# Optimization experiments

Hardware: AMD Instinct MI355X
Metric: run time of the kernel (lower is better)

Reference implementation:

```python
import jax, jax.numpy as jnp
import numpy as np

B, L, D, H = 2, 2048, 2048, 16
HD = D // H          # head_dim = 128
LAT = HD // 4        # latent_dim = 32


def setup_inputs() -> dict:
    key = jax.random.key(0)
    ks = jax.random.split(key, 16)
    def w(k, shape, fan_in):
        return jax.random.normal(k, shape, jnp.float32) / np.float32(np.sqrt(fan_in))
    x = jax.random.normal(ks[0], (B, L, D), jnp.float32)
    # RoPE frequencies, stored as (cos, sin) pairs: [L, HD//2, 2]
    inv_freq = 1.0 / (10000.0 ** (np.arange(0, HD, 2, dtype=np.float32) / HD))
    ang = np.outer(np.arange(L, dtype=np.float32), inv_freq)
    freqs_cis = jnp.stack([jnp.asarray(np.cos(ang)), jnp.asarray(np.sin(ang))], axis=-1)
    return dict(
        x=x, freqs_cis=freqs_cis,
        Wq=w(ks[1], (D, D), D), bq=jnp.zeros((D,), jnp.float32),
        Wk=w(ks[2], (D, D), D), bk=jnp.zeros((D,), jnp.float32),
        Wv=w(ks[3], (D, D), D), bv=jnp.zeros((D,), jnp.float32),
        Wqc=w(ks[4], (LAT, HD), HD), bqc=jnp.zeros((LAT,), jnp.float32),
        Wkc=w(ks[5], (LAT, HD), HD), bkc=jnp.zeros((LAT,), jnp.float32),
        Wvc=w(ks[6], (LAT, HD), HD), bvc=jnp.zeros((LAT,), jnp.float32),
        Wd=w(ks[7], (HD, LAT), LAT), bd=jnp.zeros((HD,), jnp.float32),
        Wo=w(ks[8], (D, D), D), bo=jnp.zeros((D,), jnp.float32),
    )


def _rope(t, freqs_cis):
    # t: [B,H,L,HD]; freqs_cis: [L, HD//2, 2] (cos, sin)
    tp = t.reshape(t.shape[:-1] + (HD // 2, 2))
    a, b = tp[..., 0], tp[..., 1]
    cr = freqs_cis[:, :, 0]  # [L, HD//2]
    ci = freqs_cis[:, :, 1]
    ra = a * cr - b * ci
    rb = a * ci + b * cr
    return jnp.stack([ra, rb], axis=-1).reshape(t.shape)


def reference(x, freqs_cis, Wq, bq, Wk, bk, Wv, bv, Wqc, bqc, Wkc, bkc, Wvc, bvc, Wd, bd, Wo, bo):
    Bx, Lx, Dx = x.shape
    # QKV projections -> [B,H,L,HD]
    def proj(W, bias):
        return (x @ W.T + bias).reshape(Bx, Lx, H, HD).transpose(0, 2, 1, 3)
    q = proj(Wq, bq)
    k = proj(Wk, bk)
    v = proj(Wv, bv)
    q = _rope(q, freqs_cis)
    k = _rope(k, freqs_cis)
    # per-head compression to latent dim: [B,H,L,LAT]
    qc = q @ Wqc.T + bqc
    kc = k @ Wkc.T + bkc
    vc = v @ Wvc.T + bvc
    scores = jnp.einsum('bhie,bhje->bhij', qc, kc) / np.float32(np.sqrt(LAT))
    mask = jnp.triu(jnp.ones((Lx, Lx), bool), 1)  # future positions
    scores = jnp.where(mask, jnp.float32(-jnp.inf), scores)
    probs = jax.nn.softmax(scores, axis=-1)
    attn = jnp.einsum('bhij,bhje->bhie', probs, vc)  # [B,H,L,LAT]
    attn = attn @ Wd.T + bd                          # decompress -> [B,H,L,HD]
    attn = attn.transpose(0, 2, 1, 3).reshape(Bx, Lx, Dx)
    return attn @ Wo.T + bo
```

## Files before the change

### kernel.cpp

```cpp
#include <hip/hip_runtime.h>

typedef __attribute__((ext_vector_type(8))) __bf16 bf16x8;
typedef __attribute__((ext_vector_type(4))) __bf16 bf16x4;
typedef __attribute__((ext_vector_type(4))) float f32x4;
typedef __attribute__((ext_vector_type(16))) float f32x16;

#define LL 2048
#define DD 2048
#define HH 16
#define HDIM 128

__global__ __launch_bounds__(256)
void cvt_all(const float* __restrict__ x, const float* __restrict__ Wq,
             const float* __restrict__ Wk, const float* __restrict__ Wqc,
             const float* __restrict__ Wkc,
             __bf16* __restrict__ xb, __bf16* __restrict__ Wqb, __bf16* __restrict__ Wkb,
             __bf16* __restrict__ Wqcb, __bf16* __restrict__ Wkcb)
{
    size_t i = (size_t)blockIdx.x * 256 + threadIdx.x;
    const float* s; __bf16* d; size_t off;
    if (i < 2097152)      { s = x;   d = xb;   off = i; }
    else if (i < 3145728) { s = Wq;  d = Wqb;  off = i - 2097152; }
    else if (i < 4194304) { s = Wk;  d = Wkb;  off = i - 3145728; }
    else if (i < 4195328) { s = Wqc; d = Wqcb; off = i - 4194304; }
    else                  { s = Wkc; d = Wkcb; off = i - 4195328; }
    float4 v = *(const float4*)(s + off * 4);
    bf16x4 o = { (__bf16)v.x, (__bf16)v.y, (__bf16)v.z, (__bf16)v.w };
    *(bf16x4*)(d + off * 4) = o;
}

__global__ __launch_bounds__(256)
void build_wv_eff(const float* __restrict__ Wv, const float* __restrict__ Wvc,
                  const float* __restrict__ bv, const float* __restrict__ bvc,
                  __bf16* __restrict__ Wveff, float* __restrict__ bveff)
{
    __shared__ float WvcT[128][32];
    const int h = blockIdx.x, dc = blockIdx.y, tid = threadIdx.x;
    for (int i = tid; i < 4096; i += 256) WvcT[i & 127][i >> 7] = Wvc[i];
    __syncthreads();
    const int d  = dc * 64 + (tid & 63);
    const int o0 = (tid >> 6) * 8;
    float acc[8] = {};
    for (int j = 0; j < 128; ++j) {
        const float w = Wv[(size_t)(h * 128 + j) * 2048 + d];
        #pragma unroll
        for (int o = 0; o < 8; ++o) acc[o] += WvcT[j][o0 + o] * w;
    }
    #pragma unroll
    for (int o = 0; o < 8; ++o)
        Wveff[(size_t)(h * 32 + o0 + o) * 2048 + d] = (__bf16)acc[o];
    if (dc == 0 && tid < 32) {
        float s = bvc[tid];
        for (int j = 0; j < 128; ++j) s += WvcT[j][tid] * bv[h * 128 + j];
        bveff[h * 32 + tid] = s;
    }
}

__global__ __launch_bounds__(256)
void build_wo_eff(const float* __restrict__ Wo, const float* __restrict__ Wd,
                  __bf16* __restrict__ Woeff)
{
    __shared__ float WdL[128][32];
    const int dc = blockIdx.x, h = blockIdx.y, tid = threadIdx.x;
    for (int i = tid; i < 4096; i += 256) WdL[i >> 5][i & 31] = Wd[i];
    __syncthreads();
    const int dout = dc * 64 + (tid & 63);
    const int o0   = (tid >> 6) * 8;
    float acc[8] = {};
    const float* wrow = Wo + (size_t)dout * 2048 + h * 128;
    for (int u = 0; u < 128; ++u) {
        const float w = wrow[u];
        #pragma unroll
        for (int o = 0; o < 8; ++o) acc[o] += WdL[u][o0 + o] * w;
    }
    #pragma unroll
    for (int o = 0; o < 8; ++o)
        Woeff[(size_t)dout * 512 + h * 32 + o0 + o] = (__bf16)acc[o];
}

__global__ __launch_bounds__(256)
void build_bo_eff(const float* __restrict__ Wo, const float* __restrict__ bd,
                  const float* __restrict__ bo, float* __restrict__ boeff)
{
    __shared__ float bdL[128];
    const int tid = threadIdx.x;
    if (tid < 128) bdL[tid] = bd[tid];
    __syncthreads();
    const int d  = blockIdx.x * 32 + (tid >> 3);
    const int s0 = (tid & 7) * 64;
    float s = 0.f;
    const float* wrow = Wo + (size_t)d * 2048 + s0 * 4;
    for (int c4 = 0; c4 < 64; ++c4) {
        float4 wv = *(const float4*)(wrow + c4 * 4);
        const int cb = ((s0 + c4) * 4) & 127;
        s += wv.x * bdL[cb] + wv.y * bdL[cb + 1] + wv.z * bdL[cb + 2] + wv.w * bdL[cb + 3];
    }
    #pragma unroll
    for (int off = 4; off; off >>= 1) s += __shfl_down(s, off, 8);
    if ((tid & 7) == 0) boeff[d] = bo[d] + s;
}

typedef unsigned int u32;
typedef const __attribute__((address_space(1))) u32* gp_t;
typedef __attribute__((address_space(3))) u32* lp_t;
__device__ __forceinline__ void gload16(const __bf16* g, __bf16* l)
{
    __builtin_amdgcn_global_load_lds((gp_t)(const void*)g, (lp_t)(void*)l, 16, 0, 0);
}

#define MF16(a, b, c) __builtin_amdgcn_mfma_f32_16x16x32_bf16(a, b, c, 0, 0, 0)

__global__ __launch_bounds__(512, 2)
void gemm_qkv8(const __bf16* __restrict__ A,
               const __bf16* __restrict__ Wq, const __bf16* __restrict__ Wk,
               const __bf16* __restrict__ Wveff,
               const float* __restrict__ bq, const float* __restrict__ bk,
               const float* __restrict__ bveff,
               __bf16* __restrict__ qb, __bf16* __restrict__ kb, __bf16* __restrict__ vt)
{
    __shared__ __bf16 lds[2][4][8192];

    const int bid = blockIdx.x;
    const int xcd = bid & 7;
    const int jj  = bid >> 3;
    const int by  = xcd * 2 + (jj / 18);
    const int bx  = jj % 18;
    const int m0  = by * 256;
    const int which = (bx >= 16) ? 2 : (bx >> 3);
    const int nseg  = (which == 2) ? (bx - 16) * 256 : (bx & 7) * 256;
    const __bf16* W = which == 0 ? Wq : which == 1 ? Wk : Wveff;

    const int tid  = threadIdx.x;
    const int wid  = tid >> 6;
    const int lane = tid & 63;
    const int wr   = wid >> 2;
    const int wc   = wid & 3;
    const int l15  = lane & 15;
    const int l4   = lane >> 4;
    const int c7   = l15 & 7;
    const int slotB = 2 + (wc >> 1);
    const int rbB   = (wc & 1) * 64;

    const int r0 = tid >> 3;
    const int cs = ((tid & 7) ^ (r0 & 7)) * 8;

    const __bf16* gA0 = A + (size_t)(m0 + r0) * 2048 + cs;
    const __bf16* gB0 = W + (size_t)(nseg + r0) * 2048 + cs;

    #define STAGE_ALL(dbuf, kk)                                                \
    {                                                                          \
        __bf16* s0 = &lds[dbuf][0][wid * 512];                                 \
        __bf16* s1 = &lds[dbuf][1][wid * 512];                                 \
        __bf16* s2 = &lds[dbuf][2][wid * 512];                                 \
        __bf16* s3 = &lds[dbuf][3][wid * 512];                                 \
        gload16(gA0 + (kk), s0);                                               \
        gload16(gA0 + (size_t)64 * 2048 + (kk), s0 + 4096);                    \
        gload16(gA0 + (size_t)128 * 2048 + (kk), s1);                          \
        gload16(gA0 + (size_t)192 * 2048 + (kk), s1 + 4096);                   \
        gload16(gB0 + (kk), s2);                                               \
        gload16(gB0 + (size_t)64 * 2048 + (kk), s2 + 4096);                    \
        gload16(gB0 + (size_t)128 * 2048 + (kk), s3);                          \
        gload16(gB0 + (size_t)192 * 2048 + (kk), s3 + 4096);                   \
    }

    #define RD_A(dbuf, mf, ks) \
        (*(const bf16x8*)&lds[dbuf][wr][((mf) * 16 + l15) * 64 + ((((ks) * 4 + l4) ^ c7) * 8)])
    #define RD_B(dbuf, nf, ks) \
        (*(const bf16x8*)&lds[dbuf][slotB][(rbB + (nf) * 16 + l15) * 64 + ((((ks) * 4 + l4) ^ c7) * 8)])

    f32x4 acc[8][4] = {};

    STAGE_ALL(0, 0)
    __syncthreads();

    for (int t = 0; t < 32; ++t) {
        const int d  = t & 1;
        const int dn = d ^ 1;
        if (t < 31) STAGE_ALL(dn, (t + 1) * 64)

        #pragma unroll
        for (int ks = 0; ks < 2; ++ks) {
            bf16x8 fa[8], fb[4];
            #pragma unroll
            for (int mf = 0; mf < 8; ++mf) fa[mf] = RD_A(d, mf, ks);
            #pragma unroll
            for (int nf = 0; nf < 4; ++nf) fb[nf] = RD_B(d, nf, ks);
            __builtin_amdgcn_s_setprio(1);
            #pragma unroll
            for (int mf = 0; mf < 8; ++mf)
                #pragma unroll
                for (int nf = 0; nf < 4; ++nf)
                    acc[mf][nf] = MF16(fa[mf], fb[nf], acc[mf][nf]);
            __builtin_amdgcn_s_setprio(0);
        }
        __syncthreads();
    }
    #undef STAGE_ALL
    #undef RD_A
    #undef RD_B

    if (which < 2) {
        __bf16* C = which ? kb : qb;
        const float* bb = which ? bk : bq;
        #pragma unroll
        for (int nf = 0; nf < 4; ++nf) {
            const int col = nseg + wc * 64 + nf * 16 + l15;
            const float bv = bb[col];
            #pragma unroll
            for (int mf = 0; mf < 8; ++mf) {
                const int row0 = m0 + wr * 128 + mf * 16 + l4 * 4;
                #pragma unroll
                for (int rr = 0; rr < 4; ++rr)
                    C[(size_t)(row0 + rr) * 2048 + col] = (__bf16)(acc[mf][nf][rr] + bv);
            }
        }
    } else {
        #pragma unroll
        for (int nf = 0; nf < 4; ++nf) {
            const int ncol = nseg + wc * 64 + nf * 16 + l15;
            const float bv = bveff[ncol];
            const int hh = ncol >> 5, oo = ncol & 31;
            #pragma unroll
            for (int mf = 0; mf < 8; ++mf) {
                const int row0 = m0 + wr * 128 + mf * 16 + l4 * 4;
                const int b = row0 >> 11, l0 = row0 & 2047;
                bf16x4 pk = { (__bf16)(acc[mf][nf][0] + bv), (__bf16)(acc[mf][nf][1] + bv),
                              (__bf16)(acc[mf][nf][2] + bv), (__bf16)(acc[mf][nf][3] + bv) };
                *(bf16x4*)(vt + ((size_t)((b * 16 + hh) * 32 + oo)) * 2048 + l0) = pk;
            }
        }
    }
}

__global__ __launch_bounds__(256)
void gemm_ao(const __bf16* __restrict__ ao, const __bf16* __restrict__ Woeff,
             const float* __restrict__ boeff, float* __restrict__ out)
{
    __shared__ __bf16 As[128][64];
    __shared__ __bf16 Bs[128][64];
    const int bid = blockIdx.x;
    const int x   = bid & 7;
    const int jj  = bid >> 3;
    const int bx  = x * 2 + (jj & 1);
    const int by  = jj >> 1;
    const int m0  = by * 128;
    const int n0  = bx * 128;

    const int tid  = threadIdx.x;
    const int wave = tid >> 6;
    const int lane = tid & 63;
    const int wr   = (wave >> 1) * 64;
    const int wc   = (wave & 1) * 64;
    const int lr   = lane & 15;
    const int lk   = (lane >> 4) * 8;
    const int srow = wave * 32 + (lane >> 3);
    const int scol = (lane & 7) * 8;

    f32x4 acc[4][4] = {};
    __bf16* lA = &As[wave * 32][0];
    __bf16* lB = &Bs[wave * 32][0];
    const __bf16* Ww = Woeff + (size_t)(n0 + srow) * 512 + scol;

    for (int k0 = 0; k0 < 512; k0 += 64) {
        const int kk = k0 + scol;
        const int hblk = kk >> 5, oo = kk & 31;
        #pragma unroll
        for (int j = 0; j < 4; ++j) {
            const int r = m0 + srow + j * 8;
            const int b = r >> 11, l = r & 2047;
            gload16(ao + ((size_t)((b << 4) + hblk) * 2048 + l) * 32 + oo, lA + j * 512);
            gload16(Ww + (size_t)(j * 8) * 512 + k0, lB + j * 512);
        }
        __syncthreads();
        #pragma unroll
        for (int ks = 0; ks < 2; ++ks) {
            bf16x8 af[4], bfr[4];
            #pragma unroll
            for (int m = 0; m < 4; ++m)
                af[m] = *(const bf16x8*)(&As[wr + m * 16 + lr][ks * 32 + lk]);
            #pragma unroll
            for (int n = 0; n < 4; ++n)
                bfr[n] = *(const bf16x8*)(&Bs[wc + n * 16 + lr][ks * 32 + lk]);
            #pragma unroll
            for (int m = 0; m < 4; ++m)
                #pragma unroll
                for (int n = 0; n < 4; ++n)
                    acc[m][n] = MF16(af[m], bfr[n], acc[m][n]);
        }
        __syncthreads();
    }

    const int orow = (lane >> 4) * 4;
    #pragma unroll
    for (int n = 0; n < 4; ++n) {
        const int col = n0 + wc + n * 16 + lr;
        const float bv = boeff[col];
        #pragma unroll
        for (int m = 0; m < 4; ++m) {
            #pragma unroll
            for (int r = 0; r < 4; ++r) {
                const int row = m0 + wr + m * 16 + orow + r;
                out[(size_t)row * 2048 + col] = acc[m][n][r] + bv;
            }
        }
    }
}

__global__ __launch_bounds__(256)
void latproj_mfma(const __bf16* __restrict__ qb, const __bf16* __restrict__ kb,
                  const __bf16* __restrict__ Wqcb, const __bf16* __restrict__ Wkcb,
                  const float* __restrict__ bq, const float* __restrict__ bk,
                  const float* __restrict__ fc,
                  __bf16* __restrict__ qc, __bf16* __restrict__ kc)
{
    const int which = blockIdx.y;
    const __bf16* in = which == 0 ? qb : kb;
    const __bf16* Wb = which == 0 ? Wqcb : Wkcb;
    const float*  bs = which == 0 ? bq : bk;

    const int wave = threadIdx.x >> 6;
    const int lane = threadIdx.x & 63;
    const int o    = lane & 31;
    const int hi   = lane >> 5;
    const int g0   = (blockIdx.x * 4 + wave) * 32;

    bf16x8 wf[8];
    #pragma unroll
    for (int ks = 0; ks < 8; ++ks)
        wf[ks] = *(const bf16x8*)(Wb + o * 128 + ks * 16 + hi * 8);

    const int g = g0 + o;
    const int b = g >> 15, h = (g >> 11) & 15, l = g & (LL - 1);
    const __bf16* arow = in + ((size_t)(b * LL + l)) * DD + h * HDIM;
    const float* fcr = fc + (size_t)l * 128;

    f32x16 C = {};
    #pragma unroll
    for (int ks = 0; ks < 8; ++ks) {
        bf16x8 af = *(const bf16x8*)(arow + ks * 16 + hi * 8);
        const float4 cA = *(const float4*)(fcr + (ks * 8 + hi * 4) * 2);
        const float4 cB = *(const float4*)(fcr + (ks * 8 + hi * 4) * 2 + 4);
        float a, bb_;
        a = (float)af[0]; bb_ = (float)af[1];
        af[0] = (__bf16)(a * cA.x - bb_ * cA.y); af[1] = (__bf16)(a * cA.y + bb_ * cA.x);
        a = (float)af[2]; bb_ = (float)af[3];
        af[2] = (__bf16)(a * cA.z - bb_ * cA.w); af[3] = (__bf16)(a * cA.w + bb_ * cA.z);
        a = (float)af[4]; bb_ = (float)af[5];
        af[4] = (__bf16)(a * cB.x - bb_ * cB.y); af[5] = (__bf16)(a * cB.y + bb_ * cB.x);
        a = (float)af[6]; bb_ = (float)af[7];
        af[6] = (__bf16)(a * cB.z - bb_ * cB.w); af[7] = (__bf16)(a * cB.w + bb_ * cB.z);
        C = __builtin_amdgcn_mfma_f32_32x32x16_bf16(af, wf[ks], C, 0, 0, 0);
    }

    const float bias = bs[o];
    const float QSCALE = 0.17677669529663689f * 1.44269504088896340f;
    __bf16* outp = (which == 0 ? qc : kc);
    #pragma unroll
    for (int r = 0; r < 16; ++r) {
        const int ro = (r & 3) + 8 * (r >> 2) + 4 * hi;
        float v = C[r] + bias;
        if (which == 0) v *= QSCALE;
        outp[(size_t)(g0 + ro) * 32 + o] = (__bf16)v;
    }
}

__device__ __forceinline__ unsigned pkbf2(float a, float b)
{
    union { __bf16 h[2]; unsigned u; } x;
    x.h[0] = (__bf16)a; x.h[1] = (__bf16)b;
    return x.u;
}

#if __has_builtin(__builtin_amdgcn_permlane32_swap)
typedef unsigned int uint2v __attribute__((ext_vector_type(2)));
__device__ __forceinline__ void plswap(unsigned a, unsigned b, unsigned& w_lo, unsigned& w_hi, int)
{
    uint2v r = __builtin_amdgcn_permlane32_swap(a, b, false, false);
    w_lo = r[0]; w_hi = r[1];
}
#else
__device__ __forceinline__ void plswap(unsigned a, unsigned b, unsigned& w_lo, unsigned& w_hi, int hi)
{
    unsigned ax = (unsigned)__shfl_xor((int)a, 32);
    unsigned bx = (unsigned)__shfl_xor((int)b, 32);
    w_lo = hi ? bx : a;
    w_hi = hi ? b  : ax;
}
#endif

__global__ __launch_bounds__(64)
void attn_part(const __bf16* __restrict__ qc, const __bf16* __restrict__ kc,
               const __bf16* __restrict__ vt,
               float* __restrict__ pm, float* __restrict__ pl, float* __restrict__ po)
{
    const int id  = blockIdx.x;
    const int bhl = id & 7;
    const int c   = id >> 3;
    const int bhh = c / 160;
    const int lin = c - bhh * 160;
    int s, ci;
    if (lin < 16)      { s = lin; ci = 0; }
    else if (lin < 48) { int q = lin - 16; s = 16 + (q >> 1); ci = q & 1; }
    else if (lin < 96) { int q = lin - 48; int d = q / 3; s = 32 + d; ci = q - d * 3; }
    else               { int q = lin - 96; s = 48 + (q >> 2); ci = q & 3; }
    const int bh = bhh * 8 + bhl;

    const int lane = threadIdx.x;
    const int qcol = lane & 31;
    const int hi   = lane >> 5;

    const __bf16* qbase = qc + ((size_t)bh * LL + (size_t)s * 32) * 32;
    const __bf16* kbase = kc + (size_t)bh * LL * 32;
    const __bf16* vbase = vt + (size_t)bh * 32 * LL;

    const bf16x8 qf0 = *(const bf16x8*)(qbase + qcol * 32 + hi * 8);
    const bf16x8 qf1 = *(const bf16x8*)(qbase + qcol * 32 + 16 + hi * 8);

    float m = -1e30f, lsum = 0.f;
    f32x16 O = {};

    const int t0 = ci * 16;
    const int t1 = min(s, t0 + 15);

    const __bf16* krow = kbase + (size_t)(t0 * 32 + qcol) * 32 + hi * 8;
    const __bf16* vrow = vbase + (size_t)qcol * LL + t0 * 32 + hi * 8;
    bf16x8 kc0 = *(const bf16x8*)(krow);
    bf16x8 kc1 = *(const bf16x8*)(krow + 16);
    bf16x8 vc0 = *(const bf16x8*)(vrow);
    bf16x8 vc1 = *(const bf16x8*)(vrow + 16);

    for (int t = t0; t <= t1; ++t) {
        const int tn = (t < t1) ? t + 1 : t;
        const __bf16* krn = kbase + (size_t)(tn * 32 + qcol) * 32 + hi * 8;
        const __bf16* vrn = vbase + (size_t)qcol * LL + tn * 32 + hi * 8;
        bf16x8 kn0 = *(const bf16x8*)(krn);
        bf16x8 kn1 = *(const bf16x8*)(krn + 16);
        bf16x8 vn0 = *(const bf16x8*)(vrn);
        bf16x8 vn1 = *(const bf16x8*)(vrn + 16);

        f32x16 S = {};
        S = __builtin_amdgcn_mfma_f32_32x32x16_bf16(kc0, qf0, S, 0, 0, 0);
        S = __builtin_amdgcn_mfma_f32_32x32x16_bf16(kc1, qf1, S, 0, 0, 0);

        if (t == s) {
            #pragma unroll
            for (int r = 0; r < 16; ++r) {
                const int kl = (r & 3) + 8 * (r >> 2) + 4 * hi;
                if (kl > qcol) S[r] = -1e30f;
            }
        }
        float tm = S[0];
        #pragma unroll
        for (int r = 1; r < 16; ++r) tm = fmaxf(tm, S[r]);
        tm = fmaxf(tm, __shfl_xor(tm, 32));
        const float mn = fmaxf(m, tm);
        const float fr = exp2f(m - mn);
        m = mn;
        float p[16]; float ls = 0.f;
        #pragma unroll
        for (int r = 0; r < 16; ++r) { p[r] = exp2f(S[r] - m); ls += p[r]; }
        lsum = lsum * fr + ls;
        #pragma unroll
        for (int r = 0; r < 16; ++r) O[r] *= fr;

        unsigned w[8];
        #pragma unroll
        for (int i = 0; i < 8; ++i) w[i] = pkbf2(p[2 * i], p[2 * i + 1]);
        union PF { unsigned u[4]; bf16x8 v; } pf1, pf2;
        plswap(w[0], w[2], pf1.u[0], pf1.u[2], hi);
        plswap(w[1], w[3], pf1.u[1], pf1.u[3], hi);
        plswap(w[4], w[6], pf2.u[0], pf2.u[2], hi);
        plswap(w[5], w[7], pf2.u[1], pf2.u[3], hi);

        O = __builtin_amdgcn_mfma_f32_32x32x16_bf16(vc0, pf1.v, O, 0, 0, 0);
        O = __builtin_amdgcn_mfma_f32_32x32x16_bf16(vc1, pf2.v, O, 0, 0, 0);

        kc0 = kn0; kc1 = kn1; vc0 = vn0; vc1 = vn1;
    }

    const float L = lsum + __shfl_xor(lsum, 32);
    const size_t g = (size_t)bh * LL + (size_t)s * 32 + qcol;
    const size_t slot = g * 4 + ci;
    if (hi == 0) { pm[slot] = m; pl[slot] = L; }
    float* pp = po + slot * 32;
    #pragma unroll
    for (int g4 = 0; g4 < 4; ++g4) {
        float4 v = { O[g4 * 4 + 0], O[g4 * 4 + 1], O[g4 * 4 + 2], O[g4 * 4 + 3] };
        *(float4*)(pp + g4 * 8 + 4 * hi) = v;
    }
}

__global__ __launch_bounds__(256)
void attn_comb(const float* __restrict__ pm, const float* __restrict__ pl,
               const float* __restrict__ po, __bf16* __restrict__ ao)
{
    const int g = blockIdx.x * 256 + threadIdx.x;
    const int i = g & (LL - 1);
    const int nch = (i >> 9) + 1;
    float m = -1e30f;
    for (int c = 0; c < nch; ++c) m = fmaxf(m, pm[(size_t)g * 4 + c]);
    float L = 0.f;
    float o[32] = {};
    for (int c = 0; c < nch; ++c) {
        const float w = exp2f(pm[(size_t)g * 4 + c] - m);
        L += w * pl[(size_t)g * 4 + c];
        const float* pp = po + ((size_t)g * 4 + c) * 32;
        #pragma unroll
        for (int d4 = 0; d4 < 8; ++d4) {
            float4 v = *(const float4*)(pp + d4 * 4);
            o[d4*4+0] += w * v.x; o[d4*4+1] += w * v.y;
            o[d4*4+2] += w * v.z; o[d4*4+3] += w * v.w;
        }
    }
    const float inv = 1.f / L;
    #pragma unroll
    for (int d8 = 0; d8 < 4; ++d8) {
        bf16x8 v;
        #pragma unroll
        for (int j = 0; j < 8; ++j) v[j] = (__bf16)(o[d8 * 8 + j] * inv);
        *(bf16x8*)(ao + (size_t)g * 32 + d8 * 8) = v;
    }
}

extern "C" void kernel_launch(void* const* d_in, const int* in_sizes, int n_in,
                              void* d_out, int out_size, void* d_ws, size_t ws_size,
                              hipStream_t stream)
{
    const float* x   = (const float*)d_in[0];
    const float* fc  = (const float*)d_in[1];
    const float* Wq  = (const float*)d_in[2];
    const float* bq  = (const float*)d_in[3];
    const float* Wk  = (const float*)d_in[4];
    const float* bk  = (const float*)d_in[5];
    const float* Wv  = (const float*)d_in[6];
    const float* bv  = (const float*)d_in[7];
    const float* Wqc = (const float*)d_in[8];
    const float* bqc = (const float*)d_in[9];
    const float* Wkc = (const float*)d_in[10];
    const float* bkc = (const float*)d_in[11];
    const float* Wvc = (const float*)d_in[12];
    const float* bvc = (const float*)d_in[13];
    const float* Wd  = (const float*)d_in[14];
    const float* bd  = (const float*)d_in[15];
    const float* Wo  = (const float*)d_in[16];
    const float* bo  = (const float*)d_in[17];
    float* out = (float*)d_out;

    const size_t MB = 1048576;
    char* w = (char*)d_ws;
    __bf16* xb    = (__bf16*)(w);
    __bf16* Wqb   = (__bf16*)(w + 16 * MB);
    __bf16* Wkb   = (__bf16*)(w + 24 * MB);
    __bf16* Wveff = (__bf16*)(w + 32 * MB);
    __bf16* qb    = (__bf16*)(w + 34 * MB);
    __bf16* kb    = (__bf16*)(w + 50 * MB);
    __bf16* qcbf  = (__bf16*)(w + 66 * MB);
    __bf16* kcbf  = (__bf16*)(w + 70 * MB);
    __bf16* vtbf  = (__bf16*)(w + 74 * MB);
    __bf16* aobf  = (__bf16*)(w + 78 * MB);
    __bf16* Wqcb  = (__bf16*)(w + 82 * MB);
    __bf16* Wkcb  = (__bf16*)(w + 82 * MB + 8192);
    __bf16* Woeff = (__bf16*)(w + 83 * MB);
    float*  boeff = (float*)(w + 85 * MB);
    float*  bveff = (float*)(w + 85 * MB + 8192);

    float* po = (float*)d_ws;
    float* pm = (float*)(w + 32 * MB);
    float* pl = (float*)(w + 33 * MB);

    if (ws_size < (size_t)90 * MB) return;

    cvt_all<<<16392, 256, 0, stream>>>(x, Wq, Wk, Wqc, Wkc, xb, Wqb, Wkb, Wqcb, Wkcb);
    build_wv_eff<<<dim3(16, 32), 256, 0, stream>>>(Wv, Wvc, bv, bvc, Wveff, bveff);
    build_wo_eff<<<dim3(32, 16), 256, 0, stream>>>(Wo, Wd, Woeff);
    build_bo_eff<<<64, 256, 0, stream>>>(Wo, bd, bo, boeff);

    gemm_qkv8<<<288, 512, 0, stream>>>(xb, Wqb, Wkb, Wveff, bq, bk, bveff, qb, kb, vtbf);

    latproj_mfma<<<dim3(512, 2), 256, 0, stream>>>(qb, kb, Wqcb, Wkcb, bqc, bkc, fc,
                                                   qcbf, kcbf);

    attn_part<<<5120, 64, 0, stream>>>(qcbf, kcbf, vtbf, pm, pl, po);
    attn_comb<<<256, 256, 0, stream>>>(pm, pl, po, aobf);

    gemm_ao<<<512, 256, 0, stream>>>(aobf, Woeff, boeff, out);
}
```

Before: 253.2 us.

## Use four-stage LDS ring with BK=32 and split stage issue in QKV GEMM

```diff
diff --git a/kernel.cpp b/kernel.cpp
--- a/kernel.cpp
+++ b/kernel.cpp
@@ -118,7 +118,7 @@
                const float* __restrict__ bveff,
                __bf16* __restrict__ qb, __bf16* __restrict__ kb, __bf16* __restrict__ vt)
 {
-    __shared__ __bf16 lds[2][4][8192];
+    __shared__ __bf16 lds[4][2][8192];
 
     const int bid = blockIdx.x;
     const int xcd = bid & 7;
@@ -137,65 +137,75 @@
     const int wc   = wid & 3;
     const int l15  = lane & 15;
     const int l4   = lane >> 4;
-    const int c7   = l15 & 7;
-    const int slotB = 2 + (wc >> 1);
-    const int rbB   = (wc & 1) * 64;
-
-    const int r0 = tid >> 3;
-    const int cs = ((tid & 7) ^ (r0 & 7)) * 8;
-
-    const __bf16* gA0 = A + (size_t)(m0 + r0) * 2048 + cs;
-    const __bf16* gB0 = W + (size_t)(nseg + r0) * 2048 + cs;
-
-    #define STAGE_ALL(dbuf, kk)                                                \
-    {                                                                          \
-        __bf16* s0 = &lds[dbuf][0][wid * 512];                                 \
-        __bf16* s1 = &lds[dbuf][1][wid * 512];                                 \
-        __bf16* s2 = &lds[dbuf][2][wid * 512];                                 \
-        __bf16* s3 = &lds[dbuf][3][wid * 512];                                 \
-        gload16(gA0 + (kk), s0);                                               \
-        gload16(gA0 + (size_t)64 * 2048 + (kk), s0 + 4096);                    \
-        gload16(gA0 + (size_t)128 * 2048 + (kk), s1);                          \
-        gload16(gA0 + (size_t)192 * 2048 + (kk), s1 + 4096);                   \
-        gload16(gB0 + (kk), s2);                                               \
-        gload16(gB0 + (size_t)64 * 2048 + (kk), s2 + 4096);                    \
-        gload16(gB0 + (size_t)128 * 2048 + (kk), s3);                          \
-        gload16(gB0 + (size_t)192 * 2048 + (kk), s3 + 4096);                   \
-    }
-
-    #define RD_A(dbuf, mf, ks) \
-        (*(const bf16x8*)&lds[dbuf][wr][((mf) * 16 + l15) * 64 + ((((ks) * 4 + l4) ^ c7) * 8)])
-    #define RD_B(dbuf, nf, ks) \
-        (*(const bf16x8*)&lds[dbuf][slotB][(rbB + (nf) * 16 + l15) * 64 + ((((ks) * 4 + l4) ^ c7) * 8)])
+    const int swz  = (l4 ^ (l15 & 3)) * 8;
+
+    const int srl  = lane >> 2;
+    const int scol = ((lane & 3) ^ (srl & 3)) * 8;
+    const __bf16* gA0 = A + (size_t)(m0 + wid * 32 + srl) * 2048 + scol;
+    const __bf16* gA1 = gA0 + (size_t)16 * 2048;
+    const __bf16* gB0 = W + (size_t)(nseg + wid * 32 + srl) * 2048 + scol;
+    const __bf16* gB1 = gB0 + (size_t)16 * 2048;
+
+    #define STAGE_A(bb, kkv)                                           \
+    {   __bf16* d_ = &lds[bb][0][(wid * 2) * 512];                     \
+        gload16(gA0 + (kkv), d_);                                      \
+        gload16(gA1 + (kkv), d_ + 512);                                \
+    }
+    #define STAGE_B(bb, kkv)                                           \
+    {   __bf16* d_ = &lds[bb][1][(wid * 2) * 512];                     \
+        gload16(gB0 + (kkv), d_);                                      \
+        gload16(gB1 + (kkv), d_ + 512);                                \
+    }
+    #define RD_A(bb, mf) (*(const bf16x8*)&lds[bb][0][(wr * 128 + (mf) * 16 + l15) * 32 + swz])
+    #define RD_B(bb, nf) (*(const bf16x8*)&lds[bb][1][(wc * 64 + (nf) * 16 + l15) * 32 + swz])
 
     f32x4 acc[8][4] = {};
 
-    STAGE_ALL(0, 0)
-    __syncthreads();
-
-    for (int t = 0; t < 32; ++t) {
-        const int d  = t & 1;
-        const int dn = d ^ 1;
-        if (t < 31) STAGE_ALL(dn, (t + 1) * 64)
-
-        #pragma unroll
-        for (int ks = 0; ks < 2; ++ks) {
-            bf16x8 fa[8], fb[4];
-            #pragma unroll
-            for (int mf = 0; mf < 8; ++mf) fa[mf] = RD_A(d, mf, ks);
-            #pragma unroll
-            for (int nf = 0; nf < 4; ++nf) fb[nf] = RD_B(d, nf, ks);
-            __builtin_amdgcn_s_setprio(1);
-            #pragma unroll
-            for (int mf = 0; mf < 8; ++mf)
-                #pragma unroll
-                for (int nf = 0; nf < 4; ++nf)
-                    acc[mf][nf] = MF16(fa[mf], fb[nf], acc[mf][nf]);
-            __builtin_amdgcn_s_setprio(0);
-        }
-        __syncthreads();
-    }
-    #undef STAGE_ALL
+    STAGE_A(0, 0)  STAGE_B(0, 0)
+    STAGE_A(1, 32) STAGE_B(1, 32)
+    STAGE_A(2, 64) STAGE_B(2, 64)
+
+    #define TILE_BODY(bb, VMS, DOSTAGE, kkv)                                  \
+    {                                                                         \
+        const int b_ = (bb);                                                  \
+        asm volatile("s_waitcnt vmcnt(" VMS ")" ::: "memory");                \
+        __builtin_amdgcn_s_barrier();                                         \
+        bf16x8 fa[8], fb[4];                                                  \
+        _Pragma("unroll")                                                     \
+        for (int mf = 0; mf < 8; ++mf) fa[mf] = RD_A(b_, mf);                 \
+        fb[0] = RD_B(b_, 0); fb[1] = RD_B(b_, 1);                             \
+        if (DOSTAGE) STAGE_A(((b_ + 3) & 3), (kkv))                           \
+        asm volatile("s_waitcnt lgkmcnt(0)" ::: "memory");                    \
+        __builtin_amdgcn_sched_barrier(0);                                    \
+        __builtin_amdgcn_s_setprio(1);                                        \
+        _Pragma("unroll")                                                     \
+        for (int mf = 0; mf < 8; ++mf) {                                      \
+            acc[mf][0] = MF16(fa[mf], fb[0], acc[mf][0]);                     \
+            acc[mf][1] = MF16(fa[mf], fb[1], acc[mf][1]);                     \
+        }                                                                     \
+        __builtin_amdgcn_s_setprio(0);                                        \
+        fb[2] = RD_B(b_, 2); fb[3] = RD_B(b_, 3);                             \
+        if (DOSTAGE) STAGE_B(((b_ + 3) & 3), (kkv))                           \
+        asm volatile("s_waitcnt lgkmcnt(0)" ::: "memory");                    \
+        __builtin_amdgcn_sched_barrier(0);                                    \
+        __builtin_amdgcn_s_setprio(1);                                        \
+        _Pragma("unroll")                                                     \
+        for (int mf = 0; mf < 8; ++mf) {                                      \
+            acc[mf][2] = MF16(fa[mf], fb[2], acc[mf][2]);                     \
+            acc[mf][3] = MF16(fa[mf], fb[3], acc[mf][3]);                     \
+        }                                                                     \
+        __builtin_amdgcn_s_setprio(0);                                        \
+    }
+
+    for (int t = 0; t < 61; ++t)
+        TILE_BODY((t & 3), "8", true, (t + 3) * 32)
+    TILE_BODY(1, "8", false, 0)
+    TILE_BODY(2, "4", false, 0)
+    TILE_BODY(3, "0", false, 0)
+
+    #undef TILE_BODY
+    #undef STAGE_A
+    #undef STAGE_B
     #undef RD_A
     #undef RD_B
 
```

Result: no change. 258.2 us (+2.0%).
